# Kernel optimization log

Measured on AMD Instinct MI355X. Metric: run time of the kernel, lower is better.

The kernel has to match this reference:

```python
import jax, jax.numpy as jnp
import numpy as np

DIM = 1024
HEADS = 16
DIM_HEAD = 64
INNER = HEADS * DIM_HEAD
THETA = 10000.0
EPS = 1e-5


def setup_inputs() -> dict:
    key = jax.random.key(0)
    k1, k2, k3, k4 = jax.random.split(key, 4)
    b, n = 4, 2048
    x = jax.random.normal(k1, (b, n, DIM), dtype=jnp.float32)
    gamma = jnp.ones((DIM,), jnp.float32)
    beta = jnp.zeros((DIM,), jnp.float32)
    w_qkv = jax.random.normal(k2, (DIM, 3 * INNER), dtype=jnp.float32) * (DIM ** -0.5)
    w_out = jax.random.normal(k3, (INNER, DIM), dtype=jnp.float32) * (INNER ** -0.5)
    b_out = jax.random.normal(k4, (DIM,), dtype=jnp.float32) * 0.01
    return {"x": x, "gamma": gamma, "beta": beta, "w_qkv": w_qkv, "w_out": w_out, "b_out": b_out}


def _rope_cos_sin(n, d, dtype):
    # freqs_cis = exp(i * t * theta^{-2j/d}) for j in [0, d/2)
    inv = 1.0 / (THETA ** (jnp.arange(0, d, 2, dtype=jnp.float32) / d))  # (d/2,)
    ang = jnp.arange(n, dtype=jnp.float32)[:, None] * inv[None, :]       # (n, d/2)
    return jnp.cos(ang).astype(dtype), jnp.sin(ang).astype(dtype)


def _apply_rope(t, cos, sin):
    # t: (b, n, h, d); rotate adjacent pairs along d
    b, n, h, d = t.shape
    tr = t.reshape(b, n, h, d // 2, 2)
    e, o = tr[..., 0], tr[..., 1]
    c = cos[None, :, None, :]
    s = sin[None, :, None, :]
    out = jnp.stack([e * c - o * s, e * s + o * c], axis=-1)
    return out.reshape(b, n, h, d)


def reference(x, gamma, beta, w_qkv, w_out, b_out):
    b, n, _ = x.shape
    # LayerNorm
    mu = jnp.mean(x, axis=-1, keepdims=True)
    var = jnp.mean(jnp.square(x - mu), axis=-1, keepdims=True)
    xn = (x - mu) * jax.lax.rsqrt(var + EPS) * gamma + beta
    # QKV projection (no bias)
    qkv = xn @ w_qkv  # (b, n, 3*INNER)
    q, k, v = jnp.split(qkv, 3, axis=-1)
    q = q.reshape(b, n, HEADS, DIM_HEAD)
    k = k.reshape(b, n, HEADS, DIM_HEAD)
    v = v.reshape(b, n, HEADS, DIM_HEAD)
    # RoPE on q, k (per head, global_start_pos = 0)
    cos, sin = _rope_cos_sin(n, DIM_HEAD, x.dtype)
    q = _apply_rope(q, cos, sin)
    k = _apply_rope(k, cos, sin)
    # attention
    scale = DIM_HEAD ** -0.5
    dots = jnp.einsum('bnhd,bmhd->bhnm', q, k) * scale
    attn = jax.nn.softmax(dots, axis=-1)
    out = jnp.einsum('bhnm,bmhd->bnhd', attn, v).reshape(b, n, INNER)
    return out @ w_out + b_out
```

## Files before the change

kernel.cpp:

```cpp
#include <hip/hip_runtime.h>
#include <hip/hip_fp16.h>

typedef __attribute__((ext_vector_type(8))) short short8;
typedef __attribute__((ext_vector_type(4))) short short4v;
typedef __attribute__((ext_vector_type(4))) float floatx4;
typedef _Float16 half8 __attribute__((ext_vector_type(8)));

static __device__ __forceinline__ short f2h(float f) {
    _Float16 h = (_Float16)f;
    return __builtin_bit_cast(short, h);
}

static __device__ __forceinline__ floatx4 mfma16(short8 a, short8 b, floatx4 c) {
    return __builtin_amdgcn_mfma_f32_16x16x32_f16(__builtin_bit_cast(half8, a),
                                                  __builtin_bit_cast(half8, b), c, 0, 0, 0);
}

static __device__ __forceinline__ void async16(const void* g, void* l) {
    __builtin_amdgcn_global_load_lds((const __attribute__((address_space(1))) void*)g,
                                     (__attribute__((address_space(3))) void*)l, 16, 0, 0);
}

__global__ __launch_bounds__(256) void ln_kernel(const float* __restrict__ x,
                                                 const float* __restrict__ gamma,
                                                 const float* __restrict__ beta,
                                                 short* __restrict__ xh) {
    __shared__ float red[8];
    const int row = blockIdx.x, tid = threadIdx.x;
    const int w = tid >> 6, lane = tid & 63;
    const float4 v = ((const float4*)(x + (size_t)row * 1024))[tid];
    float s = v.x + v.y + v.z + v.w;
    float ss = v.x * v.x + v.y * v.y + v.z * v.z + v.w * v.w;
#pragma unroll
    for (int off = 32; off; off >>= 1) {
        s += __shfl_xor(s, off);
        ss += __shfl_xor(ss, off);
    }
    if (lane == 0) { red[w] = s; red[4 + w] = ss; }
    __syncthreads();
    s = red[0] + red[1] + red[2] + red[3];
    ss = red[4] + red[5] + red[6] + red[7];
    const float mu = s * (1.f / 1024.f);
    const float rs = rsqrtf(ss * (1.f / 1024.f) - mu * mu + 1e-5f);
    const float4 g = ((const float4*)gamma)[tid];
    const float4 bt = ((const float4*)beta)[tid];
    short4v ph;
    ph[0] = f2h((v.x - mu) * rs * g.x + bt.x);
    ph[1] = f2h((v.y - mu) * rs * g.y + bt.y);
    ph[2] = f2h((v.z - mu) * rs * g.z + bt.z);
    ph[3] = f2h((v.w - mu) * rs * g.w + bt.w);
    *(short4v*)(xh + (size_t)row * 1024 + tid * 4) = ph;
}

__global__ void tcast_h(const float* __restrict__ in, short* __restrict__ out, int R, int C) {
    __shared__ float t[32][33];
    const int bx = blockIdx.x * 32, by = blockIdx.y * 32;
    const int tx = threadIdx.x, ty = threadIdx.y;
#pragma unroll
    for (int i = 0; i < 32; i += 8) t[ty + i][tx] = in[(size_t)(by + ty + i) * C + bx + tx];
    __syncthreads();
#pragma unroll
    for (int i = 0; i < 32; i += 8) out[(size_t)(bx + ty + i) * R + by + tx] = f2h(t[tx][ty + i]);
}

__global__ __launch_bounds__(256, 2) void gemm_qkv(const short* __restrict__ A,
                                                   const short* __restrict__ BT,
                                                   short* __restrict__ Qd, short* __restrict__ Kd,
                                                   short* __restrict__ VTb) {
    extern __shared__ __align__(16) short pool[];
    short* sA = pool;
    short* sB = pool + 4096;
    short* sOut = pool;

    const int tid = threadIdx.x;
    const int w = tid >> 6, lane = tid & 63, quad = lane >> 4, l15 = lane & 15;
    const int wm = w >> 1, wn = w & 1;
    const int m0 = blockIdx.y * 128, n0 = blockIdx.x * 128;

    floatx4 acc[4][4];
#pragma unroll
    for (int i = 0; i < 4; i++)
#pragma unroll
        for (int j = 0; j < 4; j++) acc[i][j] = (floatx4){0.f, 0.f, 0.f, 0.f};

    for (int k0 = 0; k0 < 1024; k0 += 32) {
        __syncthreads();
#pragma unroll
        for (int i = 0; i < 2; ++i) {
            int c = i * 256 + tid;
            int r = c >> 2, kc = (c & 3) << 3;
            async16(A + (size_t)(m0 + r) * 1024 + k0 + kc, (char*)sA + c * 16);
            async16(BT + (size_t)(n0 + r) * 1024 + k0 + kc, (char*)sB + c * 16);
        }
        __syncthreads();
        short8 af[4], bf[4];
#pragma unroll
        for (int t = 0; t < 4; t++) {
            af[t] = *(const short8*)(sA + (wm * 64 + t * 16 + l15) * 32 + quad * 8);
            bf[t] = *(const short8*)(sB + (wn * 64 + t * 16 + l15) * 32 + quad * 8);
        }
#pragma unroll
        for (int tm = 0; tm < 4; tm++)
#pragma unroll
            for (int tn = 0; tn < 4; tn++) acc[tm][tn] = mfma16(af[tm], bf[tn], acc[tm][tn]);
    }

    __syncthreads();

    const int b = m0 >> 11, nnb = m0 & 2047;
    const bool isV = (n0 >= 2048);
    if (!isV) {
        const float qs = (n0 < 1024) ? 0.18033688011112042f : 1.0f;
#pragma unroll
        for (int tn = 0; tn < 4; tn++) {
            const int d = tn * 16 + l15;
            const int colL = wn * 64 + tn * 16 + l15;
            const float inv = exp2f((float)(d >> 1) * -0.4152410118609203f);
#pragma unroll
            for (int tm = 0; tm < 4; tm++) {
                const int rowL = wm * 64 + tm * 16 + quad * 4;
#pragma unroll
                for (int i = 0; i < 4; i++) {
                    float v = acc[tm][tn][i];
                    float pv = __shfl_xor(v, 1);
                    float ang = (float)(nnb + rowL + i) * inv;
                    float sn = __sinf(ang), cs = __cosf(ang);
                    float r = (d & 1) ? (pv * sn + v * cs) : (v * cs - pv * sn);
                    sOut[(rowL + i) * 136 + colL] = f2h(r * qs);
                }
            }
        }
        __syncthreads();
        short* dst0 = (n0 < 1024) ? Qd : Kd;
        const int hbase = (n0 & 1023) >> 6;
#pragma unroll
        for (int it = 0; it < 8; ++it) {
            int c = it * 256 + tid;
            int r = c >> 4, cg = (c & 15) * 8;
            int h = hbase + (cg >> 6), d = cg & 63;
            *(short8*)(dst0 + ((size_t)((b * 16 + h) * 2048 + nnb + r)) * 64 + d) =
                *(const short8*)(sOut + r * 136 + cg);
        }
    } else {
#pragma unroll
        for (int tn = 0; tn < 4; tn++) {
            const int colL = wn * 64 + tn * 16 + l15;
#pragma unroll
            for (int tm = 0; tm < 4; tm++) {
                const int rowL = wm * 64 + tm * 16 + quad * 4;
#pragma unroll
                for (int i = 0; i < 4; i++)
                    sOut[colL * 136 + rowL + i] = f2h(acc[tm][tn][i]);
            }
        }
        __syncthreads();
        const int hbase = (n0 & 1023) >> 6;
#pragma unroll
        for (int it = 0; it < 8; ++it) {
            int c = it * 256 + tid;
            int ci = c >> 4, rg = (c & 15) * 8;
            int h = hbase + (ci >> 6), d = ci & 63;
            *(short8*)(VTb + ((size_t)((b * 16 + h) * 64 + d)) * 2048 + nnb + rg) =
                *(const short8*)(sOut + ci * 136 + rg);
        }
    }
}

__global__ __launch_bounds__(256, 2) void gemm_out(const short* __restrict__ A,
                                                   const short* __restrict__ BT,
                                                   float* __restrict__ Fout,
                                                   const float* __restrict__ bias) {
    __shared__ __align__(16) short sA[128 * 32];
    __shared__ __align__(16) short sB[128 * 32];
    const int tid = threadIdx.x;
    const int w = tid >> 6, lane = tid & 63, quad = lane >> 4, l15 = lane & 15;
    const int wm = w >> 1, wn = w & 1;
    const int m0 = blockIdx.y * 128, n0 = blockIdx.x * 128;

    floatx4 acc[4][4];
#pragma unroll
    for (int i = 0; i < 4; i++)
#pragma unroll
        for (int j = 0; j < 4; j++) acc[i][j] = (floatx4){0.f, 0.f, 0.f, 0.f};

    for (int k0 = 0; k0 < 1024; k0 += 32) {
        __syncthreads();
#pragma unroll
        for (int i = 0; i < 2; ++i) {
            int c = i * 256 + tid;
            int r = c >> 2, kc = (c & 3) << 3;
            async16(A + (size_t)(m0 + r) * 1024 + k0 + kc, (char*)sA + c * 16);
            async16(BT + (size_t)(n0 + r) * 1024 + k0 + kc, (char*)sB + c * 16);
        }
        __syncthreads();
        short8 af[4], bf[4];
#pragma unroll
        for (int t = 0; t < 4; t++) af[t] = *(const short8*)(sA + (wm * 64 + t * 16 + l15) * 32 + quad * 8);
#pragma unroll
        for (int t = 0; t < 4; t++) bf[t] = *(const short8*)(sB + (wn * 64 + t * 16 + l15) * 32 + quad * 8);
#pragma unroll
        for (int tm = 0; tm < 4; tm++)
#pragma unroll
            for (int tn = 0; tn < 4; tn++) acc[tm][tn] = mfma16(af[tm], bf[tn], acc[tm][tn]);
    }

#pragma unroll
    for (int tn = 0; tn < 4; tn++) {
        const int col = n0 + wn * 64 + tn * 16 + l15;
        const float bb = bias[col];
#pragma unroll
        for (int tm = 0; tm < 4; tm++) {
            const int row0 = m0 + wm * 64 + tm * 16 + quad * 4;
#pragma unroll
            for (int i = 0; i < 4; i++) Fout[(size_t)(row0 + i) * 1024 + col] = acc[tm][tn][i] + bb;
        }
    }
}

__global__ __launch_bounds__(512, 4) void attn_kernel(const short* __restrict__ Qg,
                                                      const short* __restrict__ Kg,
                                                      const short* __restrict__ VTg,
                                                      short* __restrict__ Og) {
    extern __shared__ __align__(16) short apool[];
    short* sKV0 = apool;
    short* sKV1 = apool + 8192;
    short* sP = apool + 16384;

    const int tid = threadIdx.x;
    const int w = tid >> 6, lane = tid & 63, quad = lane >> 4, l15 = lane & 15;
    const int qt = blockIdx.x, bh = blockIdx.y;

    const short* Qp = Qg + (size_t)(bh * 2048 + qt * 256) * 64;
    const short* Kp = Kg + (size_t)bh * 2048 * 64;
    const short* Vp = VTg + (size_t)bh * 64 * 2048;

    const int str = tid >> 3, stc = tid & 7;
    const int scl = stc ^ (str & 7);
    const int kSrcOff = str * 64 + scl * 8;
    const int vSrcOff = str * 2048 + scl * 8;
    const int dstOff = tid * 16;

    short8 aq[2][2];
#pragma unroll
    for (int rb = 0; rb < 2; rb++)
#pragma unroll
        for (int kh = 0; kh < 2; kh++)
            aq[rb][kh] = *(const short8*)(Qp + (w * 32 + rb * 16 + l15) * 64 + kh * 32 + quad * 8);

    short8 ones;
#pragma unroll
    for (int j = 0; j < 8; j++) ones[j] = 0x3C00;

    floatx4 o4[2][4], ol[2];
#pragma unroll
    for (int rb = 0; rb < 2; rb++) {
#pragma unroll
        for (int dt = 0; dt < 4; dt++) o4[rb][dt] = (floatx4){0.f, 0.f, 0.f, 0.f};
        ol[rb] = (floatx4){0.f, 0.f, 0.f, 0.f};
    }

    async16(Kp + kSrcOff, (char*)sKV0 + dstOff);
    async16(Vp + vSrcOff, (char*)(sKV0 + 4096) + dstOff);

    const int swz0 = (quad ^ (l15 & 7)) << 3;
    const int swz1 = ((4 | quad) ^ (l15 & 7)) << 3;

    for (int kt = 0; kt < 32; ++kt) {
        const short* sK = (kt & 1) ? sKV1 : sKV0;
        const short* sVT = sK + 4096;
        __syncthreads();
        if (kt + 1 < 32) {
            short* nK = (kt & 1) ? sKV0 : sKV1;
            const int n0 = (kt + 1) * 64;
            async16(Kp + (size_t)n0 * 64 + kSrcOff, (char*)nK + dstOff);
            async16(Vp + n0 + vSrcOff, (char*)(nK + 4096) + dstOff);
        }

#pragma unroll
        for (int tn = 0; tn < 4; tn++) {
            const int rbase = (tn * 16 + l15) * 64;
            short8 b0 = *(const short8*)(sK + rbase + swz0);
            short8 b1 = *(const short8*)(sK + rbase + swz1);
#pragma unroll
            for (int rb = 0; rb < 2; rb++) {
                floatx4 z = (floatx4){0.f, 0.f, 0.f, 0.f};
                z = mfma16(aq[rb][0], b0, z);
                z = mfma16(aq[rb][1], b1, z);
                const int qb = w * 32 + rb * 16 + quad * 4;
                const int phys = (((tn << 1) | (l15 >> 3)) ^ ((qb >> 2) & 7)) << 3;
                short* pw = sP + qb * 64 + phys + (l15 & 7);
#pragma unroll
                for (int i = 0; i < 4; i++) pw[i * 64] = f2h(exp2f(z[i]));
            }
        }
        __syncthreads();

#pragma unroll
        for (int nc = 0; nc < 2; nc++) {
            const int csw = (nc << 2) | quad;
            short8 pa[4];
#pragma unroll
            for (int dt = 0; dt < 4; dt++)
                pa[dt] = *(const short8*)(sVT + (dt * 16 + l15) * 64 + ((csw ^ (l15 & 7)) << 3));
#pragma unroll
            for (int rb = 0; rb < 2; rb++) {
                const int q = w * 32 + rb * 16 + l15;
                short8 pb = *(const short8*)(sP + q * 64 + ((csw ^ ((q >> 2) & 7)) << 3));
#pragma unroll
                for (int dt = 0; dt < 4; dt++) o4[rb][dt] = mfma16(pa[dt], pb, o4[rb][dt]);
                ol[rb] = mfma16(ones, pb, ol[rb]);
            }
        }
    }

    float linv[2];
    linv[0] = 1.0f / ol[0][0];
    linv[1] = 1.0f / ol[1][0];

    __syncthreads();
    short* sO = sP;
#pragma unroll
    for (int rb = 0; rb < 2; rb++) {
        const int q = w * 32 + rb * 16 + l15;
#pragma unroll
        for (int dt = 0; dt < 4; dt++) {
            short4v pk;
#pragma unroll
            for (int i = 0; i < 4; i++) pk[i] = f2h(o4[rb][dt][i] * linv[rb]);
            const int d0 = dt * 16 + quad * 4;
            *(short4v*)(sO + q * 64 + (((d0 >> 3) ^ (q & 7)) << 3) + (d0 & 7)) = pk;
        }
    }
    __syncthreads();
    const int b = bh >> 4, h = bh & 15;
#pragma unroll
    for (int it = 0; it < 4; ++it) {
        int g = it * 512 + tid;
        int r = g >> 3, c = g & 7;
        *(short8*)(Og + (size_t)(b * 2048 + qt * 256 + r) * 1024 + h * 64 + c * 8) =
            *(const short8*)(sO + r * 64 + ((c ^ (r & 7)) << 3));
    }
}

extern "C" void kernel_launch(void* const* d_in, const int* in_sizes, int n_in, void* d_out,
                              int out_size, void* d_ws, size_t ws_size, hipStream_t stream) {
    const float* x = (const float*)d_in[0];
    const float* gamma = (const float*)d_in[1];
    const float* beta = (const float*)d_in[2];
    const float* w_qkv = (const float*)d_in[3];
    const float* w_out = (const float*)d_in[4];
    const float* b_out = (const float*)d_in[5];
    float* out = (float*)d_out;

    char* ws = (char*)d_ws;
    short* xh = (short*)ws;
    short* wqkvT = (short*)(ws + 16777216);
    short* woT = (short*)(ws + 23068672);
    short* VTb = (short*)(ws + 25165824);
    short* Qd = (short*)d_out;
    short* Kd = (short*)d_out + 8388608;

    ln_kernel<<<8192, 256, 0, stream>>>(x, gamma, beta, xh);
    tcast_h<<<dim3(96, 32), dim3(32, 8), 0, stream>>>(w_qkv, wqkvT, 1024, 3072);
    tcast_h<<<dim3(32, 32), dim3(32, 8), 0, stream>>>(w_out, woT, 1024, 1024);
    gemm_qkv<<<dim3(24, 64), 256, 34816, stream>>>(xh, wqkvT, Qd, Kd, VTb);
    attn_kernel<<<dim3(8, 64), 512, 65536, stream>>>(Qd, Kd, VTb, xh);
    gemm_out<<<dim3(8, 64), 256, 0, stream>>>(xh, woT, out, b_out);
}
```

Before: 311.9 us.

## Keep attention probabilities in registers instead of staging through LDS

```diff
diff --git a/kernel.cpp b/kernel.cpp
--- a/kernel.cpp
+++ b/kernel.cpp
@@ -5,10 +5,17 @@
 typedef __attribute__((ext_vector_type(4))) short short4v;
 typedef __attribute__((ext_vector_type(4))) float floatx4;
 typedef _Float16 half8 __attribute__((ext_vector_type(8)));
+typedef __fp16 fp16x2 __attribute__((ext_vector_type(2)));
+typedef __attribute__((ext_vector_type(4))) unsigned uintx4;
 
 static __device__ __forceinline__ short f2h(float f) {
     _Float16 h = (_Float16)f;
     return __builtin_bit_cast(short, h);
+}
+
+static __device__ __forceinline__ unsigned pkrtz(float a, float b) {
+    fp16x2 h = __builtin_amdgcn_cvt_pkrtz(a, b);
+    return __builtin_bit_cast(unsigned, h);
 }
 
 static __device__ __forceinline__ floatx4 mfma16(short8 a, short8 b, floatx4 c) {
@@ -224,7 +231,6 @@
     extern __shared__ __align__(16) short apool[];
     short* sKV0 = apool;
     short* sKV1 = apool + 8192;
-    short* sP = apool + 16384;
 
     const int tid = threadIdx.x;
     const int w = tid >> 6, lane = tid & 63, quad = lane >> 4, l15 = lane & 15;
@@ -277,35 +283,54 @@
         }
 
 #pragma unroll
-        for (int tn = 0; tn < 4; tn++) {
-            const int rbase = (tn * 16 + l15) * 64;
-            short8 b0 = *(const short8*)(sK + rbase + swz0);
-            short8 b1 = *(const short8*)(sK + rbase + swz1);
+        for (int nc = 0; nc < 2; nc++) {
+            floatx4 zA[2], zB[2];
+            {
+                const int rbase = ((2 * nc) * 16 + l15) * 64;
+                short8 k0 = *(const short8*)(sK + rbase + swz0);
+                short8 k1 = *(const short8*)(sK + rbase + swz1);
+#pragma unroll
+                for (int rb = 0; rb < 2; rb++) {
+                    floatx4 z = (floatx4){0.f, 0.f, 0.f, 0.f};
+                    z = mfma16(k0, aq[rb][0], z);
+                    z = mfma16(k1, aq[rb][1], z);
+                    zA[rb] = z;
+                }
+            }
+            {
+                const int rbase = ((2 * nc + 1) * 16 + l15) * 64;
+                short8 k0 = *(const short8*)(sK + rbase + swz0);
+                short8 k1 = *(const short8*)(sK + rbase + swz1);
+#pragma unroll
+                for (int rb = 0; rb < 2; rb++) {
+                    floatx4 z = (floatx4){0.f, 0.f, 0.f, 0.f};
+                    z = mfma16(k0, aq[rb][0], z);
+                    z = mfma16(k1, aq[rb][1], z);
+                    zB[rb] = z;
+                }
+            }
+
+            short8 pa[4];
+            const int r7 = l15 & 7;
+            const int h4 = (quad & 1) << 2;
+            const int cLo = (((nc << 2) | (quad >> 1)) ^ r7) << 3;
+            const int cHi = ((((nc << 2) + 2) | (quad >> 1)) ^ r7) << 3;
+#pragma unroll
+            for (int dt = 0; dt < 4; dt++) {
+                const short* rowp = sVT + (dt * 16 + l15) * 64;
+                short4v lo = *(const short4v*)(rowp + cLo + h4);
+                short4v hi = *(const short4v*)(rowp + cHi + h4);
+                pa[dt] = __builtin_shufflevector(lo, hi, 0, 1, 2, 3, 4, 5, 6, 7);
+            }
+
 #pragma unroll
             for (int rb = 0; rb < 2; rb++) {
-                floatx4 z = (floatx4){0.f, 0.f, 0.f, 0.f};
-                z = mfma16(aq[rb][0], b0, z);
-                z = mfma16(aq[rb][1], b1, z);
-                const int qb = w * 32 + rb * 16 + quad * 4;
-                const int phys = (((tn << 1) | (l15 >> 3)) ^ ((qb >> 2) & 7)) << 3;
-                short* pw = sP + qb * 64 + phys + (l15 & 7);
-#pragma unroll
-                for (int i = 0; i < 4; i++) pw[i * 64] = f2h(exp2f(z[i]));
-            }
-        }
-        __syncthreads();
-
-#pragma unroll
-        for (int nc = 0; nc < 2; nc++) {
-            const int csw = (nc << 2) | quad;
-            short8 pa[4];
-#pragma unroll
-            for (int dt = 0; dt < 4; dt++)
-                pa[dt] = *(const short8*)(sVT + (dt * 16 + l15) * 64 + ((csw ^ (l15 & 7)) << 3));
-#pragma unroll
-            for (int rb = 0; rb < 2; rb++) {
-                const int q = w * 32 + rb * 16 + l15;
-                short8 pb = *(const short8*)(sP + q * 64 + ((csw ^ ((q >> 2) & 7)) << 3));
+                uintx4 pbw;
+                pbw.x = pkrtz(exp2f(zA[rb][0]), exp2f(zA[rb][1]));
+                pbw.y = pkrtz(exp2f(zA[rb][2]), exp2f(zA[rb][3]));
+                pbw.z = pkrtz(exp2f(zB[rb][0]), exp2f(zB[rb][1]));
+                pbw.w = pkrtz(exp2f(zB[rb][2]), exp2f(zB[rb][3]));
+                short8 pb = __builtin_bit_cast(short8, pbw);
 #pragma unroll
                 for (int dt = 0; dt < 4; dt++) o4[rb][dt] = mfma16(pa[dt], pb, o4[rb][dt]);
                 ol[rb] = mfma16(ones, pb, ol[rb]);
@@ -318,7 +343,7 @@
     linv[1] = 1.0f / ol[1][0];
 
     __syncthreads();
-    short* sO = sP;
+    short* sO = apool;
 #pragma unroll
     for (int rb = 0; rb < 2; rb++) {
         const int q = w * 32 + rb * 16 + l15;
@@ -364,6 +389,6 @@
     tcast_h<<<dim3(96, 32), dim3(32, 8), 0, stream>>>(w_qkv, wqkvT, 1024, 3072);
     tcast_h<<<dim3(32, 32), dim3(32, 8), 0, stream>>>(w_out, woT, 1024, 1024);
     gemm_qkv<<<dim3(24, 64), 256, 34816, stream>>>(xh, wqkvT, Qd, Kd, VTb);
-    attn_kernel<<<dim3(8, 64), 512, 65536, stream>>>(Qd, Kd, VTb, xh);
+    attn_kernel<<<dim3(8, 64), 512, 32768, stream>>>(Qd, Kd, VTb, xh);
     gemm_out<<<dim3(8, 64), 256, 0, stream>>>(xh, woT, out, b_out);
 }
```

Measured after the change: 307.2 us. About the same (-1.5%).
